# Kernel optimization log

Hardware: AMD Instinct MI355X
Metric: run time of the kernel (lower is better)

The kernel has to match this reference:

```python
import jax, jax.numpy as jnp
import numpy as np
import math

B, T, H, NH, L = 8, 1024, 192, 2, 6
FFN, K, VOCAB, OUT, WIN = 768, 3, 256, 192, 4
KC = H // NH  # per-head channels


def _get_rel(emb, t):
    pad = max(t - (WIN + 1), 0)
    start = max(WIN + 1 - t, 0)
    p = jnp.pad(emb, ((pad, pad), (0, 0)))
    return p[start:start + 2 * t - 1]


def _rel_to_abs(x):
    # [b,h,l,2l-1] -> [b,h,l,l]
    b, h, l, _ = x.shape
    x = jnp.pad(x, ((0, 0), (0, 0), (0, 0), (0, 1)))
    xf = x.reshape(b, h, l * 2 * l)
    xf = jnp.pad(xf, ((0, 0), (0, 0), (0, l - 1)))
    return xf.reshape(b, h, l + 1, 2 * l - 1)[:, :, :l, l - 1:]


def _abs_to_rel(x):
    # [b,h,l,l] -> [b,h,l,2l-1]
    b, h, l, _ = x.shape
    x = jnp.pad(x, ((0, 0), (0, 0), (0, 0), (0, l - 1)))
    xf = x.reshape(b, h, l * (2 * l - 1))
    xf = jnp.pad(xf, ((0, 0), (0, 0), (l, 0)))
    return xf.reshape(b, h, l, 2 * l)[:, :, :, 1:]


def _ln(x, g, b):
    # channels-first LayerNorm over axis 1, x: [B,C,T]
    m = jnp.mean(x, 1, keepdims=True)
    v = jnp.var(x, 1, keepdims=True)
    return (x - m) * jax.lax.rsqrt(v + 1e-5) * g[:, None] + b[:, None]


def _conv1d(x, w, b):
    y = jax.lax.conv_general_dilated(x, w, (1,), 'SAME', dimension_numbers=('NCH', 'OIH', 'NCH'))
    return y + b[:, None]


def _attn(x, attn_mask, qw, qb, kw, kb, vw, vb, ow, ob, rel_k, rel_v):
    b, d, t = x.shape
    def proj(w, bb):
        y = jnp.einsum('oc,bct->bot', w, x) + bb[:, None]
        return y.reshape(b, NH, KC, t).transpose(0, 1, 3, 2)  # [b,h,t,kc]
    q, k, v = proj(qw, qb), proj(kw, kb), proj(vw, vb)
    qs = q / math.sqrt(KC)
    scores = jnp.einsum('bhtk,bhsk->bhts', qs, k)
    scores = scores + _rel_to_abs(jnp.einsum('bhtk,mk->bhtm', qs, _get_rel(rel_k, t)))
    scores = jnp.where(attn_mask == 0, -1e4, scores)
    p = jax.nn.softmax(scores, axis=-1)
    o = jnp.einsum('bhts,bhsk->bhtk', p, v)
    o = o + jnp.einsum('bhtm,mk->bhtk', _abs_to_rel(p), _get_rel(rel_v, t))
    o = o.transpose(0, 1, 3, 2).reshape(b, d, t)
    return jnp.einsum('oc,bct->bot', ow, o) + ob[:, None]


def setup_inputs():
    key = jax.random.key(0)
    ks = iter(jax.random.split(key, 40))
    def nrm(shape, scale):
        return jax.random.normal(next(ks), shape, jnp.float32) * scale
    w = 0.05
    inp = {
        'tokens': jax.random.randint(next(ks), (B, T), 0, VOCAB),
        'x_lengths': jax.random.randint(next(ks), (B,), T // 2, T + 1),
        'emb': nrm((VOCAB, H), H ** -0.5),
        'qw': nrm((L, H, H), w), 'qb': jnp.zeros((L, H)),
        'kw': nrm((L, H, H), w), 'kb': jnp.zeros((L, H)),
        'vw': nrm((L, H, H), w), 'vb': jnp.zeros((L, H)),
        'ow': nrm((L, H, H), w), 'ob': jnp.zeros((L, H)),
        'rel_k': nrm((L, 2 * WIN + 1, KC), KC ** -0.5),
        'rel_v': nrm((L, 2 * WIN + 1, KC), KC ** -0.5),
        'ln1_g': jnp.ones((L, H)), 'ln1_b': jnp.zeros((L, H)),
        'f1w': nrm((L, FFN, H, K), w), 'f1b': jnp.zeros((L, FFN)),
        'f2w': nrm((L, H, FFN, K), w), 'f2b': jnp.zeros((L, H)),
        'ln2_g': jnp.ones((L, H)), 'ln2_b': jnp.zeros((L, H)),
        'pw': nrm((2 * OUT, H), w), 'pb': jnp.zeros((2 * OUT,)),
        'eps': jax.random.normal(next(ks), (B, OUT, T), jnp.float32),
    }
    return inp


def reference(tokens, x_lengths, emb, qw, qb, kw, kb, vw, vb, ow, ob, rel_k, rel_v,
              ln1_g, ln1_b, f1w, f1b, f2w, f2b, ln2_g, ln2_b, pw, pb, eps):
    x = emb[tokens].transpose(0, 2, 1) * math.sqrt(H)  # [B,H,T]
    x_mask = (jnp.arange(T) < x_lengths[:, None]).astype(x.dtype)[:, None, :]  # [B,1,T]
    attn_mask = x_mask[:, :, None, :] * x_mask[:, :, :, None]  # [B,1,T,T]
    x = x * x_mask
    for i in range(L):
        y = _attn(x, attn_mask, qw[i], qb[i], kw[i], kb[i], vw[i], vb[i], ow[i], ob[i], rel_k[i], rel_v[i])
        x = _ln(x + y, ln1_g[i], ln1_b[i])
        y = jax.nn.relu(_conv1d(x * x_mask, f1w[i], f1b[i]))
        y = _conv1d(y * x_mask, f2w[i], f2b[i]) * x_mask
        x = _ln(x + y, ln2_g[i], ln2_b[i])
    x = x * x_mask
    stats = (jnp.einsum('oc,bct->bot', pw, x) + pb[:, None]) * x_mask
    m, logs = stats[:, :OUT], stats[:, OUT:]
    z = m + eps * jnp.exp(logs) * x_mask
    return (z, m, logs, x, x_mask)
```

## Files before the change

kernel.cpp:

```cpp
#include <hip/hip_runtime.h>
#include <math.h>

#define BN 8
#define TN 1024
#define HN 192
#define NHN 2
#define KCN 96
#define LN 6
#define FFNN 768
#define OUTN 192
#define QSTR 104
#define GSTR 200
#define M0S 12.0f

typedef short bfrag __attribute__((ext_vector_type(8)));
typedef float f32x4 __attribute__((ext_vector_type(4)));

__device__ __forceinline__ short f2bf(float f) {
    union { float f; unsigned u; } v; v.f = f;
    unsigned r = v.u + 0x7fffu + ((v.u >> 16) & 1u);
    return (short)(r >> 16);
}
__device__ __forceinline__ float bf2f(short s) {
    union { unsigned u; float f; } v;
    v.u = ((unsigned)(unsigned short)s) << 16;
    return v.f;
}
__device__ __forceinline__ int pack2(float a, float b) {
    return (int)(unsigned short)f2bf(a) | (((int)(unsigned short)f2bf(b)) << 16);
}

#define QSCALE 0.10206207261596575f

__global__ void k_cvt(const float* __restrict__ src, short* __restrict__ dst, int n) {
    int i = blockIdx.x * 256 + threadIdx.x;
    if (i < n) dst[i] = f2bf(src[i]);
}
__global__ void k_cvtconv(const float* __restrict__ src, short* __restrict__ dst,
                          int M, int Cin, int n) {
    int i = blockIdx.x * 256 + threadIdx.x;
    if (i >= n) return;
    int tap = i % 3;
    int c = (i / 3) % Cin;
    int m = (i / (3 * Cin)) % M;
    int l = i / (3 * Cin * M);
    dst[(((size_t)l * 3 + tap) * M + m) * Cin + c] = f2bf(src[i]);
}
__global__ void k_cvt_qkv(const float* __restrict__ qw, const float* __restrict__ kw,
                          const float* __restrict__ vw, short* __restrict__ dst, int n) {
    int i = blockIdx.x * 256 + threadIdx.x;
    if (i >= n) return;
    int c = i % 192;
    int r = (i / 192) % 576;
    int l = i / (192 * 576);
    float val, sc = 1.f;
    if (r < 192) { val = qw[((size_t)l * 192 + r) * 192 + c]; sc = QSCALE; }
    else if (r < 384) val = kw[((size_t)l * 192 + (r - 192)) * 192 + c];
    else val = vw[((size_t)l * 192 + (r - 384)) * 192 + c];
    dst[i] = f2bf(val * sc);
}
__global__ void k_cvt_qkvb(const float* __restrict__ qb, const float* __restrict__ kb,
                           const float* __restrict__ vb, float* __restrict__ dst, int n) {
    int i = blockIdx.x * 256 + threadIdx.x;
    if (i >= n) return;
    int r = i % 576;
    int l = i / 576;
    dst[i] = (r < 192) ? qb[l * 192 + r] * QSCALE
           : (r < 384) ? kb[l * 192 + r - 192]
                       : vb[l * 192 + r - 384];
}

__global__ __launch_bounds__(256) void k_embed(const int* __restrict__ tok,
        const int* __restrict__ lens, const float* __restrict__ emb,
        float* __restrict__ x, short* __restrict__ xb) {
    __shared__ float s[HN][65];
    const int b = blockIdx.y, t0 = blockIdx.x * 64, tid = threadIdx.x;
    const int len = lens[b];
    for (int idx = tid; idx < 64 * HN; idx += 256) {
        int tt = idx / HN, c = idx % HN;
        int t = t0 + tt;
        float v = 0.f;
        if (t < len) v = emb[tok[b * TN + t] * HN + c] * 13.856406460551018f;
        s[c][tt] = v;
    }
    __syncthreads();
    for (int idx = tid; idx < 64 * HN; idx += 256) {
        int c = idx >> 6, tt = idx & 63;
        x[((size_t)b * HN + c) * TN + t0 + tt] = s[c][tt];
    }
    for (int idx = tid; idx < 64 * 96; idx += 256) {
        int tt = idx / 96, p = idx % 96;
        ((int*)xb)[((size_t)(b * TN + t0 + tt)) * 96 + p] = pack2(s[2 * p][tt], s[2 * p + 1][tt]);
    }
}

template <bool MERGE, bool MASK_OUT>
__global__ __launch_bounds__(256) void k_g192(
        const short* __restrict__ W, const short* __restrict__ X,
        const float* __restrict__ bias, float* __restrict__ Y,
        const short* __restrict__ accP, const float* __restrict__ lPp,
        const int* __restrict__ lens, int M) {
    __shared__ short Wt[64 * GSTR];
    __shared__ short Xt[64 * GSTR];
    __shared__ float linv[128];
    const int b = blockIdx.z, m0 = blockIdx.y * 64, t0 = blockIdx.x * 64;
    const int len = lens[b];
    const int tid = threadIdx.x;
    const int w = tid >> 6, lane = tid & 63, col = lane & 15, quad = lane >> 4;

    if (MERGE) {
        if (tid < 128) {
            int tt = tid & 63, h = tid >> 6;
            float l = 0.f;
#pragma unroll
            for (int sh = 0; sh < 4; ++sh)
                l += lPp[(((size_t)sh * BN + b) * NHN + h) * TN + t0 + tt];
            linv[tid] = (l > 0.f) ? 1.f / l : 0.f;
        }
        __syncthreads();
    }
    for (int i = tid; i < 1536; i += 256) {
        int mm = i / 24, part = i % 24;
        *(int4*)(Wt + mm * GSTR + part * 8) =
            *(const int4*)(W + ((size_t)(m0 + mm)) * 192 + part * 8);
    }
    for (int i = tid; i < 1536; i += 256) {
        int tt = i / 24, part = i % 24;
        if (!MERGE) {
            *(int4*)(Xt + tt * GSTR + part * 8) =
                *(const int4*)(X + ((size_t)(b * TN + t0 + tt)) * 192 + part * 8);
        } else {
            const size_t base = ((size_t)(b * TN + t0 + tt)) * 192 + part * 8;
            const size_t HSq = (size_t)BN * TN * HN;
            float a[8];
#pragma unroll
            for (int c = 0; c < 8; ++c) a[c] = 0.f;
#pragma unroll
            for (int sh = 0; sh < 4; ++sh) {
                int4 v = *(const int4*)(accP + sh * HSq + base);
                const short* sv = (const short*)&v;
#pragma unroll
                for (int c = 0; c < 8; ++c) a[c] += bf2f(sv[c]);
            }
            float li = linv[(part >= 12 ? 64 : 0) + tt];
            int4 o;
            int* oi = (int*)&o;
#pragma unroll
            for (int c = 0; c < 4; ++c) oi[c] = pack2(a[2 * c] * li, a[2 * c + 1] * li);
            *(int4*)(Xt + tt * GSTR + part * 8) = o;
        }
    }
    __syncthreads();

    f32x4 acc[4];
#pragma unroll
    for (int st = 0; st < 4; ++st) acc[st] = (f32x4){0.f, 0.f, 0.f, 0.f};
#pragma unroll
    for (int ks = 0; ks < 6; ++ks) {
        bfrag af = *(const bfrag*)(Wt + (w * 16 + col) * GSTR + ks * 32 + quad * 8);
#pragma unroll
        for (int st = 0; st < 4; ++st) {
            bfrag bf = *(const bfrag*)(Xt + (st * 16 + col) * GSTR + ks * 32 + quad * 8);
            acc[st] = __builtin_amdgcn_mfma_f32_16x16x32_bf16(af, bf, acc[st], 0, 0, 0);
        }
    }

    const int mbase = m0 + w * 16 + quad * 4;
    float bs[4];
#pragma unroll
    for (int reg = 0; reg < 4; ++reg) bs[reg] = bias[mbase + reg];
#pragma unroll
    for (int st = 0; st < 4; ++st) {
        int t = t0 + st * 16 + col;
        bool om = MASK_OUT && (t >= len);
#pragma unroll
        for (int reg = 0; reg < 4; ++reg) {
            float u = acc[st][reg] + bs[reg];
            if (om) u = 0.f;
            Y[((size_t)b * M + mbase + reg) * TN + t] = u;
        }
    }
}

__global__ __launch_bounds__(256) void k_qkv2(
        const short* __restrict__ W, const short* __restrict__ X,
        const float* __restrict__ bias, short* __restrict__ qo,
        short* __restrict__ ko, short* __restrict__ vo) {
    __shared__ short Wt[64 * GSTR];
    __shared__ short Xt[64 * GSTR];
    const int b = blockIdx.z, m0 = blockIdx.y * 64, t0 = blockIdx.x * 64;
    const int tid = threadIdx.x;
    const int w = tid >> 6, lane = tid & 63, col = lane & 15, quad = lane >> 4;

    for (int i = tid; i < 1536; i += 256) {
        int mm = i / 24, part = i % 24;
        *(int4*)(Wt + mm * GSTR + part * 8) =
            *(const int4*)(W + ((size_t)(m0 + mm)) * 192 + part * 8);
    }
    for (int i = tid; i < 1536; i += 256) {
        int tt = i / 24, part = i % 24;
        *(int4*)(Xt + tt * GSTR + part * 8) =
            *(const int4*)(X + ((size_t)(b * TN + t0 + tt)) * 192 + part * 8);
    }
    __syncthreads();

    f32x4 acc[4];
#pragma unroll
    for (int st = 0; st < 4; ++st) acc[st] = (f32x4){0.f, 0.f, 0.f, 0.f};
#pragma unroll
    for (int ks = 0; ks < 6; ++ks) {
        bfrag af = *(const bfrag*)(Wt + (w * 16 + col) * GSTR + ks * 32 + quad * 8);
#pragma unroll
        for (int st = 0; st < 4; ++st) {
            bfrag bf = *(const bfrag*)(Xt + (st * 16 + col) * GSTR + ks * 32 + quad * 8);
            acc[st] = __builtin_amdgcn_mfma_f32_16x16x32_bf16(af, bf, acc[st], 0, 0, 0);
        }
    }

    const int mbase = m0 + w * 16 + quad * 4;
    const int proj = m0 / 192;
    const int mloc = mbase - proj * 192;
    float bs[4];
#pragma unroll
    for (int reg = 0; reg < 4; ++reg) bs[reg] = bias[mbase + reg];
#pragma unroll
    for (int st = 0; st < 4; ++st) {
        int t = t0 + st * 16 + col;
        float v[4];
#pragma unroll
        for (int reg = 0; reg < 4; ++reg) v[reg] = acc[st][reg] + bs[reg];
        if (proj < 2) {
            short* dst = (proj == 0) ? qo : ko;
            int2 pk;
            pk.x = pack2(v[0], v[1]);
            pk.y = pack2(v[2], v[3]);
            *(int2*)(dst + ((size_t)(b * TN + t)) * 192 + mloc) = pk;
        } else {
#pragma unroll
            for (int reg = 0; reg < 4; ++reg)
                vo[((size_t)b * 192 + mloc + reg) * TN + t] = f2bf(v[reg]);
        }
    }
}

template <int TAPS, int TT, bool RELU, bool MASK_OUT, int OUTK, int KSPLIT>
__global__ __launch_bounds__(256) void k_mgemm(
        const short* __restrict__ W, const short* __restrict__ X,
        const float* __restrict__ bias, void* __restrict__ Yv,
        float* __restrict__ Yv2, float* __restrict__ Yv3,
        const int* __restrict__ lens, int M, int Cin) {
    constexpr int P = (TAPS - 1) / 2;
    constexpr int NST = TT / 16;
    __shared__ short Wt[TAPS][64][72];
    __shared__ short Xt[TT + 2 * P][72];

    const int b = blockIdx.z;
    const int mtiles = gridDim.y / KSPLIT;
    const int kg = blockIdx.y / mtiles;
    const int m0 = (blockIdx.y % mtiles) * 64;
    const int t0 = blockIdx.x * TT;
    const int len = lens[b];
    const int tid = threadIdx.x;
    const int w = tid >> 6;
    const int lane = tid & 63;
    const int col = lane & 15;
    const int quad = lane >> 4;

    f32x4 acc[NST];
#pragma unroll
    for (int st = 0; st < NST; ++st) acc[st] = (f32x4){0.f, 0.f, 0.f, 0.f};

    const int cspan = Cin / KSPLIT;
    const int cbeg = kg * cspan;
    const int cend = cbeg + cspan;
    for (int c0 = cbeg; c0 < cend; c0 += 64) {
        __syncthreads();
        for (int i = tid; i < TAPS * 64 * 8; i += 256) {
            int tap = i / (64 * 8);
            int mm = (i / 8) & 63;
            int part = i & 7;
            *(int4*)(&Wt[tap][mm][part * 8]) =
                *(const int4*)(W + ((size_t)tap * M + m0 + mm) * Cin + c0 + part * 8);
        }
        for (int i = tid; i < (TT + 2 * P) * 8; i += 256) {
            int tt = i >> 3;
            int part = i & 7;
            int t = t0 + tt - P;
            int4 v = {0, 0, 0, 0};
            if (t >= 0 && t < TN)
                v = *(const int4*)(X + ((size_t)b * TN + t) * Cin + c0 + part * 8);
            *(int4*)(&Xt[tt][part * 8]) = v;
        }
        __syncthreads();
#pragma unroll
        for (int ks = 0; ks < 2; ++ks) {
#pragma unroll
            for (int tap = 0; tap < TAPS; ++tap) {
                bfrag af = *(const bfrag*)(&Wt[tap][w * 16 + col][ks * 32 + quad * 8]);
#pragma unroll
                for (int st = 0; st < NST; ++st) {
                    bfrag bf = *(const bfrag*)(&Xt[st * 16 + col + tap][ks * 32 + quad * 8]);
                    acc[st] = __builtin_amdgcn_mfma_f32_16x16x32_bf16(af, bf, acc[st], 0, 0, 0);
                }
            }
        }
    }

    const int mbase = m0 + w * 16 + quad * 4;
    float bs[4];
#pragma unroll
    for (int reg = 0; reg < 4; ++reg)
        bs[reg] = (KSPLIT > 1 && kg) ? 0.f : bias[mbase + reg];
#pragma unroll
    for (int st = 0; st < NST; ++st) {
        int t = t0 + st * 16 + col;
        bool om = MASK_OUT && (t >= len);
        float v[4];
#pragma unroll
        for (int reg = 0; reg < 4; ++reg) {
            float u = acc[st][reg] + bs[reg];
            if (RELU) u = fmaxf(u, 0.f);
            if (om) u = 0.f;
            v[reg] = u;
        }
        if (OUTK == 0) {
            float* dst = (KSPLIT > 1) ? (kg == 0 ? (float*)Yv : (kg == 1 ? Yv2 : Yv3))
                                      : (float*)Yv;
#pragma unroll
            for (int reg = 0; reg < 4; ++reg)
                dst[((size_t)b * M + mbase + reg) * TN + t] = v[reg];
        } else {
            int2 pk;
            pk.x = pack2(v[0], v[1]);
            pk.y = pack2(v[2], v[3]);
            *(int2*)((short*)Yv + ((size_t)(b * TN + t)) * M + mbase) = pk;
        }
    }
}

__global__ __launch_bounds__(512, 4) void k_attn4(
        const short* __restrict__ Q, const short* __restrict__ K,
        const short* __restrict__ V, const float* __restrict__ relk,
        const float* __restrict__ relv, short* __restrict__ accP,
        float* __restrict__ lP, const int* __restrict__ lens) {
    __shared__ short kt[64 * QSTR];
    __shared__ short vt[96 * 72];
    __shared__ short Pt[128 * 72];
    __shared__ short rbt[16 * QSTR];
    __shared__ float rels[128 * 12];
    __shared__ float sband[128 * 12];
    __shared__ float rvs[9 * 96];

    const int b = blockIdx.z;
    const int h = blockIdx.y >> 2, sh = blockIdx.y & 3;
    const int t0 = blockIdx.x * 128;
    const int len = lens[b];
    const int tid = threadIdx.x;
    const int w = tid >> 6;
    const int lane = tid & 63;
    const int col = lane & 15;
    const int quad = lane >> 4;

    const short* Qb = Q + ((size_t)b * TN + t0) * HN + h * KCN;
    const short* Kb = K + ((size_t)b * TN + sh * 256) * HN + h * KCN;
    const short* Vb = V + ((size_t)b * HN + h * KCN) * TN + sh * 256;

    bfrag qf[3];
#pragma unroll
    for (int ks = 0; ks < 3; ++ks)
        qf[ks] = *(const bfrag*)(Qb + (size_t)(w * 16 + col) * HN + ks * 32 + quad * 8);

    for (int i = tid; i < 9 * 96; i += 512) rvs[i] = relv[i];
    for (int i = tid; i < 16 * 96; i += 512) {
        int r = i / 96, c = i % 96;
        rbt[r * QSTR + c] = (r < 9) ? f2bf(relk[r * 96 + c]) : (short)0;
    }
    for (int i = tid; i < 128 * 12; i += 512) sband[i] = -1e30f;
    __syncthreads();

    {
        f32x4 rc = (f32x4){0.f, 0.f, 0.f, 0.f};
#pragma unroll
        for (int ks = 0; ks < 3; ++ks) {
            bfrag bf = *(const bfrag*)(rbt + col * QSTR + ks * 32 + quad * 8);
            rc = __builtin_amdgcn_mfma_f32_16x16x32_bf16(qf[ks], bf, rc, 0, 0, 0);
        }
        if (col < 12) {
#pragma unroll
            for (int reg = 0; reg < 4; ++reg)
                rels[(w * 16 + quad * 4 + reg) * 12 + col] = rc[reg];
        }
    }

    float lsum[4];
    f32x4 accv[6];
#pragma unroll
    for (int r = 0; r < 4; ++r) lsum[r] = 0.f;
#pragma unroll
    for (int n = 0; n < 6; ++n) accv[n] = (f32x4){0.f, 0.f, 0.f, 0.f};

    const int rem = len - sh * 256;
    const int nj = (rem <= 0) ? 0 : ((rem >= 256) ? 4 : ((rem + 63) >> 6));

    for (int j = 0; j < nj; ++j) {
        const int s0g = sh * 256 + j * 64;
        __syncthreads();
        for (int i = tid; i < 768; i += 512) {
            int row = i / 12, part = i % 12;
            *(int4*)(kt + row * QSTR + part * 8) =
                *(const int4*)(Kb + ((size_t)(j * 64 + row)) * HN + part * 8);
        }
        for (int i = tid; i < 768; i += 512) {
            int c = i >> 3, part = i & 7;
            *(int4*)(vt + c * 72 + part * 8) =
                *(const int4*)(Vb + (size_t)c * TN + j * 64 + part * 8);
        }
        __syncthreads();

        f32x4 sacc[4];
#pragma unroll
        for (int st = 0; st < 4; ++st) sacc[st] = (f32x4){0.f, 0.f, 0.f, 0.f};
#pragma unroll
        for (int ks = 0; ks < 3; ++ks) {
#pragma unroll
            for (int st = 0; st < 4; ++st) {
                bfrag bf = *(const bfrag*)(kt + (st * 16 + col) * QSTR + ks * 32 + quad * 8);
                sacc[st] = __builtin_amdgcn_mfma_f32_16x16x32_bf16(qf[ks], bf, sacc[st], 0, 0, 0);
            }
        }

#pragma unroll
        for (int reg = 0; reg < 4; ++reg) {
            const int lq = w * 16 + quad * 4 + reg;
            const int qg = t0 + lq;
#pragma unroll
            for (int st = 0; st < 4; ++st) {
                int sg = s0g + st * 16 + col;
                float v = sacc[st][reg];
                int d = sg - qg + 4;
                bool inb = (d >= 0) && (d <= 8);
                if (inb) v += rels[lq * 12 + d];
                if (sg >= len) v = -1e4f;
                if (inb) sband[lq * 12 + d] = v;
                float p = __expf(v - M0S);
                lsum[reg] += p;
                Pt[lq * 72 + st * 16 + col] = f2bf(p);
            }
        }
#pragma unroll
        for (int ks = 0; ks < 2; ++ks) {
            bfrag af = *(const bfrag*)(Pt + (w * 16 + col) * 72 + ks * 32 + quad * 8);
#pragma unroll
            for (int nt = 0; nt < 6; ++nt) {
                bfrag bf = *(const bfrag*)(vt + (nt * 16 + col) * 72 + ks * 32 + quad * 8);
                accv[nt] = __builtin_amdgcn_mfma_f32_16x16x32_bf16(af, bf, accv[nt], 0, 0, 0);
            }
        }
    }

#pragma unroll
    for (int reg = 0; reg < 4; ++reg) {
        lsum[reg] += __shfl_xor(lsum[reg], 1);
        lsum[reg] += __shfl_xor(lsum[reg], 2);
        lsum[reg] += __shfl_xor(lsum[reg], 4);
        lsum[reg] += __shfl_xor(lsum[reg], 8);
    }
    __syncthreads();

    short* aout = accP + (size_t)sh * BN * TN * HN;
#pragma unroll
    for (int reg = 0; reg < 4; ++reg) {
        const int lq = w * 16 + quad * 4 + reg;
        const int qg = t0 + lq;
        float pb[9];
#pragma unroll
        for (int d = 0; d < 9; ++d)
            pb[d] = __expf(sband[lq * 12 + d] - M0S);
#pragma unroll
        for (int nt = 0; nt < 6; ++nt) {
            int c = nt * 16 + col;
            float r = accv[nt][reg];
#pragma unroll
            for (int d = 0; d < 9; ++d) r += pb[d] * rvs[d * 96 + c];
            aout[((size_t)(b * TN + qg)) * HN + h * KCN + c] = f2bf(r);
        }
        if (col == 0)
            lP[(((size_t)sh * BN + b) * NHN + h) * TN + qg] = lsum[reg];
    }
}

template <int NADD>
__global__ __launch_bounds__(256) void k_ln(float* __restrict__ x,
        const float* __restrict__ y, const float* __restrict__ y2,
        const float* __restrict__ y3, const float* __restrict__ g,
        const float* __restrict__ bb, short* __restrict__ xb,
        const int* __restrict__ lens) {
    __shared__ float s[HN][33];
    __shared__ float red1[256], red2[256];
    __shared__ float mu[32], rs[32];
    const int b = blockIdx.y;
    const int t0 = blockIdx.x * 32;
    const int tid = threadIdx.x;
    const int len = lens[b];

    for (int idx = tid; idx < HN * 32; idx += 256) {
        int c = idx >> 5, tt = idx & 31;
        size_t gi = ((size_t)b * HN + c) * TN + t0 + tt;
        float v = x[gi] + y[gi];
        if (NADD >= 2) v += y2[gi];
        if (NADD >= 3) v += y3[gi];
        s[c][tt] = v;
    }
    __syncthreads();
    int tt = tid & 31, grp = tid >> 5;
    float sum = 0.f, sum2 = 0.f;
    for (int c = grp * 24; c < grp * 24 + 24; ++c) {
        float v = s[c][tt];
        sum += v;
        sum2 += v * v;
    }
    red1[tid] = sum;
    red2[tid] = sum2;
    __syncthreads();
    if (tid < 32) {
        float tot = 0.f, tot2 = 0.f;
#pragma unroll
        for (int gg = 0; gg < 8; ++gg) { tot += red1[gg * 32 + tid]; tot2 += red2[gg * 32 + tid]; }
        float mean = tot / (float)HN;
        float var = tot2 / (float)HN - mean * mean;
        mu[tid] = mean;
        rs[tid] = rsqrtf(var + 1e-5f);
    }
    __syncthreads();
    for (int idx = tid; idx < HN * 32; idx += 256) {
        int c = idx >> 5, t2 = idx & 31;
        float v = (s[c][t2] - mu[t2]) * rs[t2] * g[c] + bb[c];
        x[((size_t)b * HN + c) * TN + t0 + t2] = v;
    }
    for (int idx = tid; idx < 32 * 96; idx += 256) {
        int t2 = idx / 96, p = idx % 96;
        int c0 = 2 * p;
        float v0 = (s[c0][t2] - mu[t2]) * rs[t2] * g[c0] + bb[c0];
        float v1 = (s[c0 + 1][t2] - mu[t2]) * rs[t2] * g[c0 + 1] + bb[c0 + 1];
        if (t0 + t2 >= len) { v0 = 0.f; v1 = 0.f; }
        ((int*)xb)[((size_t)(b * TN + t0 + t2)) * 96 + p] = pack2(v0, v1);
    }
}

__global__ void k_final(const float* __restrict__ stats, const float* __restrict__ x,
        const float* __restrict__ eps, const int* __restrict__ lens,
        float* __restrict__ out) {
    int idx = blockIdx.x * 256 + threadIdx.x;
    int t = idx % TN;
    int o = (idx / TN) % OUTN;
    int b = idx / (TN * OUTN);
    float maskv = (t < lens[b]) ? 1.f : 0.f;
    const size_t S = (size_t)BN * OUTN * TN;
    float m = stats[((size_t)(b * 2 * OUTN) + o) * TN + t];
    float ls = stats[((size_t)(b * 2 * OUTN) + OUTN + o) * TN + t];
    float e = eps[idx];
    out[idx] = m + e * expf(ls) * maskv;
    out[S + idx] = m;
    out[2 * S + idx] = ls;
    out[3 * S + idx] = x[idx] * maskv;
    if (o == 0) out[4 * S + (size_t)b * TN + t] = maskv;
}

extern "C" void kernel_launch(void* const* d_in, const int* in_sizes, int n_in,
                              void* d_out, int out_size, void* d_ws, size_t ws_size,
                              hipStream_t stream) {
    const int* tok = (const int*)d_in[0];
    const int* lens = (const int*)d_in[1];
    const float* emb = (const float*)d_in[2];
    const float* qw = (const float*)d_in[3];
    const float* qb = (const float*)d_in[4];
    const float* kw = (const float*)d_in[5];
    const float* kb = (const float*)d_in[6];
    const float* vw = (const float*)d_in[7];
    const float* vb = (const float*)d_in[8];
    const float* ow = (const float*)d_in[9];
    const float* ob = (const float*)d_in[10];
    const float* relk = (const float*)d_in[11];
    const float* relv = (const float*)d_in[12];
    const float* ln1g = (const float*)d_in[13];
    const float* ln1b = (const float*)d_in[14];
    const float* f1w = (const float*)d_in[15];
    const float* f1b = (const float*)d_in[16];
    const float* f2w = (const float*)d_in[17];
    const float* f2b = (const float*)d_in[18];
    const float* ln2g = (const float*)d_in[19];
    const float* ln2b = (const float*)d_in[20];
    const float* pw = (const float*)d_in[21];
    const float* pb = (const float*)d_in[22];
    const float* eps = (const float*)d_in[23];

    const size_t BHT = (size_t)BN * HN * TN;
    float* ws = (float*)d_ws;
    float* x = ws;
    float* yf = ws + BHT;
    short* s_xb = (short*)(ws + 2 * BHT);
    short* s_ln = (short*)(ws + 2 * BHT + BHT / 2);
    short* s_q  = (short*)(ws + 3 * BHT);
    short* s_k  = (short*)(ws + 3 * BHT + BHT / 2);
    short* s_v  = (short*)(ws + 4 * BHT);
    float* p1   = ws + 3 * BHT;
    float* p2   = ws + 4 * BHT;
    short* accP = (short*)(ws + 5 * BHT);
    short* s_y1 = (short*)(ws + 5 * BHT);
    float* stats = ws + 5 * BHT;
    short* wqkv = (short*)(ws + 7 * BHT);
    short* wo16 = wqkv + (size_t)LN * 3 * HN * HN;
    short* wp16 = wo16 + (size_t)LN * HN * HN;
    short* wf1_16 = wp16 + (size_t)2 * OUTN * HN;
    short* wf2_16 = wf1_16 + (size_t)LN * 3 * FFNN * HN;
    float* bqkv = (float*)(wf2_16 + (size_t)LN * 3 * FFNN * HN);
    float* lP = bqkv + (size_t)LN * 576;

    {
        int nq = LN * 576 * 192;
        k_cvt_qkv<<<dim3((nq + 255) / 256), 256, 0, stream>>>(qw, kw, vw, wqkv, nq);
        int nqb = LN * 576;
        k_cvt_qkvb<<<dim3((nqb + 255) / 256), 256, 0, stream>>>(qb, kb, vb, bqkv, nqb);
        int n1 = LN * HN * HN;
        k_cvt<<<dim3((n1 + 255) / 256), 256, 0, stream>>>(ow, wo16, n1);
        int n2 = 2 * OUTN * HN;
        k_cvt<<<dim3((n2 + 255) / 256), 256, 0, stream>>>(pw, wp16, n2);
        int n3 = LN * FFNN * HN * 3;
        k_cvtconv<<<dim3((n3 + 255) / 256), 256, 0, stream>>>(f1w, wf1_16, FFNN, HN, n3);
        k_cvtconv<<<dim3((n3 + 255) / 256), 256, 0, stream>>>(f2w, wf2_16, HN, FFNN, n3);
    }

    dim3 gemb(TN / 64, BN);
    k_embed<<<gemb, 256, 0, stream>>>(tok, lens, emb, x, s_xb);

    dim3 gqkv(TN / 64, 9, BN);
    dim3 gattn(TN / 128, NHN * 4, BN);
    dim3 goproj(TN / 64, HN / 64, BN);
    dim3 gf1(TN / 128, FFNN / 64, BN);
    dim3 gf2(TN / 128, 9, BN);
    dim3 gln(TN / 32, BN);

    for (int i = 0; i < LN; ++i) {
        const short* qkvwi = wqkv + (size_t)i * 576 * 192;
        const float* qkvbi = bqkv + (size_t)i * 576;
        const short* owi = wo16 + (size_t)i * HN * HN;
        const short* f1wi = wf1_16 + (size_t)i * 3 * FFNN * HN;
        const short* f2wi = wf2_16 + (size_t)i * 3 * FFNN * HN;
        const float* obi = ob + (size_t)i * HN;
        const float* rki = relk + (size_t)i * 9 * KCN;
        const float* rvi = relv + (size_t)i * 9 * KCN;
        const float* l1gi = ln1g + (size_t)i * HN;
        const float* l1bi = ln1b + (size_t)i * HN;
        const float* f1bi = f1b + (size_t)i * FFNN;
        const float* f2bi = f2b + (size_t)i * HN;
        const float* l2gi = ln2g + (size_t)i * HN;
        const float* l2bi = ln2b + (size_t)i * HN;

        k_qkv2<<<gqkv, 256, 0, stream>>>(qkvwi, s_xb, qkvbi, s_q, s_k, s_v);
        k_attn4<<<gattn, 512, 0, stream>>>(s_q, s_k, s_v, rki, rvi, accP, lP, lens);
        k_g192<true, false><<<goproj, 256, 0, stream>>>(owi, nullptr, obi, yf, accP, lP, lens, HN);
        k_ln<1><<<gln, 256, 0, stream>>>(x, yf, nullptr, nullptr, l1gi, l1bi, s_ln, lens);
        k_mgemm<3, 128, true, true, 1, 1><<<gf1, 256, 0, stream>>>(f1wi, s_ln, f1bi, s_y1, nullptr, nullptr, lens, FFNN, HN);
        k_mgemm<3, 128, false, true, 0, 3><<<gf2, 256, 0, stream>>>(f2wi, s_y1, f2bi, yf, p1, p2, lens, HN, FFNN);
        k_ln<3><<<gln, 256, 0, stream>>>(x, yf, p1, p2, l2gi, l2bi, s_xb, lens);
    }

    dim3 gstat(TN / 64, (2 * OUTN) / 64, BN);
    k_g192<false, true><<<gstat, 256, 0, stream>>>(wp16, s_xb, pb, stats, nullptr, nullptr, lens, 2 * OUTN);
    k_final<<<dim3((unsigned)(BHT / 256)), 256, 0, stream>>>(stats, x, eps, lens, (float*)d_out);
}
```

Measured before the change: 880.1 us.

## Skip compute for fully padded time tiles and fuse weight conversion kernels

After: 847.1 us. 3.7% less time.

```diff
diff --git a/kernel.cpp b/kernel.cpp
--- a/kernel.cpp
+++ b/kernel.cpp
@@ -32,42 +32,52 @@
 
 #define QSCALE 0.10206207261596575f
 
-__global__ void k_cvt(const float* __restrict__ src, short* __restrict__ dst, int n) {
+__global__ void k_cvtall(const float* __restrict__ qw, const float* __restrict__ kw,
+        const float* __restrict__ vw, const float* __restrict__ qb,
+        const float* __restrict__ kb, const float* __restrict__ vb,
+        const float* __restrict__ ow, const float* __restrict__ pw,
+        const float* __restrict__ f1w, const float* __restrict__ f2w,
+        short* __restrict__ wqkv, float* __restrict__ bqkv,
+        short* __restrict__ wo16, short* __restrict__ wp16,
+        short* __restrict__ wf1, short* __restrict__ wf2) {
+    const int N0 = LN * 576 * 192;
+    const int N1 = LN * 576;
+    const int N2 = LN * HN * HN;
+    const int N3 = 2 * OUTN * HN;
+    const int N4 = LN * FFNN * HN * 3;
     int i = blockIdx.x * 256 + threadIdx.x;
-    if (i < n) dst[i] = f2bf(src[i]);
-}
-__global__ void k_cvtconv(const float* __restrict__ src, short* __restrict__ dst,
-                          int M, int Cin, int n) {
-    int i = blockIdx.x * 256 + threadIdx.x;
-    if (i >= n) return;
-    int tap = i % 3;
-    int c = (i / 3) % Cin;
-    int m = (i / (3 * Cin)) % M;
-    int l = i / (3 * Cin * M);
-    dst[(((size_t)l * 3 + tap) * M + m) * Cin + c] = f2bf(src[i]);
-}
-__global__ void k_cvt_qkv(const float* __restrict__ qw, const float* __restrict__ kw,
-                          const float* __restrict__ vw, short* __restrict__ dst, int n) {
-    int i = blockIdx.x * 256 + threadIdx.x;
-    if (i >= n) return;
-    int c = i % 192;
-    int r = (i / 192) % 576;
-    int l = i / (192 * 576);
-    float val, sc = 1.f;
-    if (r < 192) { val = qw[((size_t)l * 192 + r) * 192 + c]; sc = QSCALE; }
-    else if (r < 384) val = kw[((size_t)l * 192 + (r - 192)) * 192 + c];
-    else val = vw[((size_t)l * 192 + (r - 384)) * 192 + c];
-    dst[i] = f2bf(val * sc);
-}
-__global__ void k_cvt_qkvb(const float* __restrict__ qb, const float* __restrict__ kb,
-                           const float* __restrict__ vb, float* __restrict__ dst, int n) {
-    int i = blockIdx.x * 256 + threadIdx.x;
-    if (i >= n) return;
-    int r = i % 576;
-    int l = i / 576;
-    dst[i] = (r < 192) ? qb[l * 192 + r] * QSCALE
-           : (r < 384) ? kb[l * 192 + r - 192]
-                       : vb[l * 192 + r - 384];
+    if (i < N0) {
+        int c = i % 192, r = (i / 192) % 576, l = i / (192 * 576);
+        float val, sc = 1.f;
+        if (r < 192) { val = qw[((size_t)l * 192 + r) * 192 + c]; sc = QSCALE; }
+        else if (r < 384) val = kw[((size_t)l * 192 + (r - 192)) * 192 + c];
+        else val = vw[((size_t)l * 192 + (r - 384)) * 192 + c];
+        wqkv[i] = f2bf(val * sc);
+        return;
+    }
+    i -= N0;
+    if (i < N1) {
+        int r = i % 576, l = i / 576;
+        bqkv[i] = (r < 192) ? qb[l * 192 + r] * QSCALE
+                : (r < 384) ? kb[l * 192 + r - 192]
+                            : vb[l * 192 + r - 384];
+        return;
+    }
+    i -= N1;
+    if (i < N2) { wo16[i] = f2bf(ow[i]); return; }
+    i -= N2;
+    if (i < N3) { wp16[i] = f2bf(pw[i]); return; }
+    i -= N3;
+    if (i < N4) {
+        int tap = i % 3, c = (i / 3) % HN, m = (i / (3 * HN)) % FFNN, l = i / (3 * HN * FFNN);
+        wf1[(((size_t)l * 3 + tap) * FFNN + m) * HN + c] = f2bf(f1w[i]);
+        return;
+    }
+    i -= N4;
+    if (i < N4) {
+        int tap = i % 3, c = (i / 3) % FFNN, m = (i / (3 * FFNN)) % HN, l = i / (3 * FFNN * HN);
+        wf2[(((size_t)l * 3 + tap) * HN + m) * FFNN + c] = f2bf(f2w[i]);
+    }
 }
 
 __global__ __launch_bounds__(256) void k_embed(const int* __restrict__ tok,
@@ -108,6 +118,20 @@
     const int tid = threadIdx.x;
     const int w = tid >> 6, lane = tid & 63, col = lane & 15, quad = lane >> 4;
 
+    if (t0 >= len) {
+        if (MASK_OUT) {
+            const int mbase = m0 + w * 16 + quad * 4;
+#pragma unroll
+            for (int st = 0; st < 4; ++st) {
+                int t = t0 + st * 16 + col;
+#pragma unroll
+                for (int reg = 0; reg < 4; ++reg)
+                    Y[((size_t)b * M + mbase + reg) * TN + t] = 0.f;
+            }
+        }
+        return;
+    }
+
     if (MERGE) {
         if (tid < 128) {
             int tt = tid & 63, h = tid >> 6;
@@ -185,12 +209,34 @@
 __global__ __launch_bounds__(256) void k_qkv2(
         const short* __restrict__ W, const short* __restrict__ X,
         const float* __restrict__ bias, short* __restrict__ qo,
-        short* __restrict__ ko, short* __restrict__ vo) {
+        short* __restrict__ ko, short* __restrict__ vo,
+        const int* __restrict__ lens) {
     __shared__ short Wt[64 * GSTR];
     __shared__ short Xt[64 * GSTR];
     const int b = blockIdx.z, m0 = blockIdx.y * 64, t0 = blockIdx.x * 64;
+    const int len = lens[b];
     const int tid = threadIdx.x;
     const int w = tid >> 6, lane = tid & 63, col = lane & 15, quad = lane >> 4;
+    const int proj = m0 / 192;
+    const int mbase = m0 + w * 16 + quad * 4;
+    const int mloc = mbase - proj * 192;
+
+    if (t0 >= len) {
+        if (proj == 1) return;
+#pragma unroll
+        for (int st = 0; st < 4; ++st) {
+            int t = t0 + st * 16 + col;
+            if (proj == 0) {
+                int2 z = {0, 0};
+                *(int2*)(qo + ((size_t)(b * TN + t)) * 192 + mloc) = z;
+            } else {
+#pragma unroll
+                for (int reg = 0; reg < 4; ++reg)
+                    vo[((size_t)b * 192 + mloc + reg) * TN + t] = 0;
+            }
+        }
+        return;
+    }
 
     for (int i = tid; i < 1536; i += 256) {
         int mm = i / 24, part = i % 24;
@@ -217,9 +263,6 @@
         }
     }
 
-    const int mbase = m0 + w * 16 + quad * 4;
-    const int proj = m0 / 192;
-    const int mloc = mbase - proj * 192;
     float bs[4];
 #pragma unroll
     for (int reg = 0; reg < 4; ++reg) bs[reg] = bias[mbase + reg];
@@ -265,6 +308,25 @@
     const int lane = tid & 63;
     const int col = lane & 15;
     const int quad = lane >> 4;
+    const int mbase = m0 + w * 16 + quad * 4;
+
+    if (MASK_OUT && t0 >= len) {
+#pragma unroll
+        for (int st = 0; st < NST; ++st) {
+            int t = t0 + st * 16 + col;
+            if (OUTK == 0) {
+                float* dst = (KSPLIT > 1) ? (kg == 0 ? (float*)Yv : (kg == 1 ? Yv2 : Yv3))
+                                          : (float*)Yv;
+#pragma unroll
+                for (int reg = 0; reg < 4; ++reg)
+                    dst[((size_t)b * M + mbase + reg) * TN + t] = 0.f;
+            } else {
+                int2 z = {0, 0};
+                *(int2*)((short*)Yv + ((size_t)(b * TN + t)) * M + mbase) = z;
+            }
+        }
+        return;
+    }
 
     f32x4 acc[NST];
 #pragma unroll
@@ -306,7 +368,6 @@
         }
     }
 
-    const int mbase = m0 + w * 16 + quad * 4;
     float bs[4];
 #pragma unroll
     for (int reg = 0; reg < 4; ++reg)
@@ -360,6 +421,12 @@
     const int lane = tid & 63;
     const int col = lane & 15;
     const int quad = lane >> 4;
+
+    if (t0 >= len) {
+        if (tid < 128)
+            lP[(((size_t)sh * BN + b) * NHN + h) * TN + t0 + tid] = 0.f;
+        return;
+    }
 
     const short* Qb = Q + ((size_t)b * TN + t0) * HN + h * KCN;
     const short* Kb = K + ((size_t)b * TN + sh * 256) * HN + h * KCN;
@@ -502,6 +569,12 @@
     const int t0 = blockIdx.x * 32;
     const int tid = threadIdx.x;
     const int len = lens[b];
+
+    if (t0 >= len) {
+        for (int idx = tid; idx < 32 * 96; idx += 256)
+            ((int*)xb)[((size_t)(b * TN + t0 + idx / 96)) * 96 + idx % 96] = 0;
+        return;
+    }
 
     for (int idx = tid; idx < HN * 32; idx += 256) {
         int c = idx >> 5, tt = idx & 31;
@@ -617,17 +690,11 @@
     float* lP = bqkv + (size_t)LN * 576;
 
     {
-        int nq = LN * 576 * 192;
-        k_cvt_qkv<<<dim3((nq + 255) / 256), 256, 0, stream>>>(qw, kw, vw, wqkv, nq);
-        int nqb = LN * 576;
-        k_cvt_qkvb<<<dim3((nqb + 255) / 256), 256, 0, stream>>>(qb, kb, vb, bqkv, nqb);
-        int n1 = LN * HN * HN;
-        k_cvt<<<dim3((n1 + 255) / 256), 256, 0, stream>>>(ow, wo16, n1);
-        int n2 = 2 * OUTN * HN;
-        k_cvt<<<dim3((n2 + 255) / 256), 256, 0, stream>>>(pw, wp16, n2);
-        int n3 = LN * FFNN * HN * 3;
-        k_cvtconv<<<dim3((n3 + 255) / 256), 256, 0, stream>>>(f1w, wf1_16, FFNN, HN, n3);
-        k_cvtconv<<<dim3((n3 + 255) / 256), 256, 0, stream>>>(f2w, wf2_16, HN, FFNN, n3);
+        long total = (long)LN * 576 * 192 + LN * 576 + LN * HN * HN + 2 * OUTN * HN
+                   + 2L * LN * FFNN * HN * 3;
+        k_cvtall<<<dim3((unsigned)((total + 255) / 256)), 256, 0, stream>>>(
+            qw, kw, vw, qb, kb, vb, ow, pw, f1w, f2w,
+            wqkv, bqkv, wo16, wp16, wf1_16, wf2_16);
     }
 
     dim3 gemb(TN / 64, BN);
@@ -656,7 +723,7 @@
         const float* l2gi = ln2g + (size_t)i * HN;
         const float* l2bi = ln2b + (size_t)i * HN;
 
-        k_qkv2<<<gqkv, 256, 0, stream>>>(qkvwi, s_xb, qkvbi, s_q, s_k, s_v);
+        k_qkv2<<<gqkv, 256, 0, stream>>>(qkvwi, s_xb, qkvbi, s_q, s_k, s_v, lens);
         k_attn4<<<gattn, 512, 0, stream>>>(s_q, s_k, s_v, rki, rvi, accP, lP, lens);
         k_g192<true, false><<<goproj, 256, 0, stream>>>(owi, nullptr, obi, yf, accP, lP, lens, HN);
         k_ln<1><<<gln, 256, 0, stream>>>(x, yf, nullptr, nullptr, l1gi, l1bi, s_ln, lens);
```
